# Kernel tuning notes

Measured on AMD Instinct MI355X. Metric: run time of the kernel, lower is better.

## Reference

```python
import jax, jax.numpy as jnp
import numpy as np

# --- configuration (matches pars / init_kwargs) ---
T, B, IN, N = 200, 256, 784, 400
ALPHA, BETA, THRESH = 0.9, 0.8, 1.0          # Synaptic neuron params
BETA_PLUS, BETA_MINUS = 0.9, 0.9             # pre / post trace decay
A_PLUS, A_MINUS = 1e-3, 1e-3                 # classic STDP amplitudes
W_MIN, W_MAX = 0.0, 1.0
LI_STRENGTH = 0.1                            # lateral inhibition strength
SPIKE_RATE = 0.05                            # input Poisson rate per step


def setup_inputs() -> dict:
    key = jax.random.key(0)
    k1, k2 = jax.random.split(key)
    # binary pre-synaptic spike train [T, B, IN]
    image = (jax.random.uniform(k1, (T, B, IN)) < SPIKE_RATE).astype(jnp.float32)
    # torch Linear default init U(-1/sqrt(IN), 1/sqrt(IN)) then clamp to [w_min, w_max]
    bound = 1.0 / np.sqrt(IN)
    W = jnp.clip(jax.random.uniform(k2, (N, IN), minval=-bound, maxval=bound), W_MIN, W_MAX)
    return {"image": image, "W": W}


def _snn_forward(image, W):
    # pre-synaptic traces: traces[0]=0, traces[t+1] = bp*traces[t] + image[t]
    # (STDP at step t uses traces[t], i.e. trace BEFORE incorporating image[t])
    pre_traces = jax.lax.scan(
        lambda tr, x: (BETA_PLUS * tr + x, tr),
        jnp.zeros_like(image[0]), image)[1]            # [T, B, IN]

    batch_ar = jnp.arange(B)

    def step(carry, xs):
        syn, mem, post, W = carry
        img_t, tr_t = xs                               # [B, IN] each
        # fc (no bias)
        cur = img_t @ W.T                              # [B, N]
        # snntorch Synaptic, reset_mechanism='subtract':
        # reset computed from incoming mem, then state update, then fire
        reset = (mem > THRESH).astype(mem.dtype)
        syn = ALPHA * syn + cur
        mem = BETA * mem + syn - reset * THRESH
        spk = (mem > THRESH).astype(mem.dtype)
        mem_rec, spk_rec = mem, spk                    # records taken here
        # lateral inhibition (winner-take-all on syn), skipped if no spikes at all
        win = jnp.argmax(spk, axis=1)                  # first spiking neuron per row
        temp = jnp.ones_like(syn).at[batch_ar, win].set(0.0)
        syn = jnp.where(jnp.sum(spk) > 0, syn - temp * LI_STRENGTH, syn)
        # post-synaptic trace update (STDP uses the UPDATED post trace)
        post = BETA_MINUS * post + spk
        # classic STDP weight update with clamp
        LTP = A_PLUS * (spk.T @ tr_t)                  # [N, IN]
        LTD = A_MINUS * (post.T @ img_t)               # [N, IN]
        W = jnp.clip(W + LTP - LTD, W_MIN, W_MAX)
        return (syn, mem, post, W), (mem_rec, spk_rec)

    zeros = jnp.zeros((B, N), dtype=image.dtype)
    init = (zeros, zeros, zeros, W)
    (_, _, _, W_final), (mem_rec, spk_rec) = jax.lax.scan(step, init, (image, pre_traces))
    return mem_rec, spk_rec, W_final


def reference(image, W):
    # returns (mem record [T,B,N], spike record [T,B,N], final weights [N,IN])
    return _snn_forward(image, W)
```

## Files before the change

### kernel.cpp

```cpp
#include <hip/hip_runtime.h>


#define T_STEPS 200
#define BATCH   256
#define INQ     784
#define NOUT    400
#define NP      512
#define GRID    256
#define NTHR    512
#define IMSZ    200704

#define OFF_WT    0
#define OFF_SYN   401920
#define OFF_MEM   532992
#define OFF_SPPO  664064
#define OFF_TRA   926208
#define OFF_TRB   1126912
#define OFF_WIN   1327616
#define OFF_FLAGS 1327872
#define OFF_BAR   1328128
#define WS_FLOATS 1332224

typedef unsigned long long ull;

__device__ __forceinline__ float ld_coh(const float* p) {
  return __hip_atomic_load(p, __ATOMIC_RELAXED, __HIP_MEMORY_SCOPE_AGENT);
}
__device__ __forceinline__ float2 ld_coh2(const float* p) {
  union { ull u; float2 f; } c;
  c.u = __hip_atomic_load((const ull*)p, __ATOMIC_RELAXED, __HIP_MEMORY_SCOPE_AGENT);
  return c.f;
}
__device__ __forceinline__ void st_coh(float* p, float v) {
  __hip_atomic_store(p, v, __ATOMIC_RELAXED, __HIP_MEMORY_SCOPE_AGENT);
}
__device__ __forceinline__ void st_coh2(float* p, float2 v) {
  union { ull u; float2 f; } c; c.f = v;
  __hip_atomic_store((ull*)p, c.u, __ATOMIC_RELAXED, __HIP_MEMORY_SCOPE_AGENT);
}

__device__ __forceinline__ void gl_lds16(const float* g, float* l) {
  __builtin_amdgcn_global_load_lds(
      (const __attribute__((address_space(1))) void*)g,
      (__attribute__((address_space(3))) void*)l, 16, 0, 0);
}
__device__ __forceinline__ void gl_lds16c(const float* g, float* l) {
  __builtin_amdgcn_global_load_lds(
      (const __attribute__((address_space(1))) void*)g,
      (__attribute__((address_space(3))) void*)l, 16, 0, 0x10);
}

__device__ __forceinline__ void gbar(unsigned* bar, unsigned k, int blk) {
  __syncthreads();
  if (threadIdx.x == 0) {
    const int g = blk >> 3;
    unsigned* garr = bar + g * 64;
    unsigned* ggen = bar + g * 64 + 32;
    unsigned* rarr = bar + 32 * 64;
    unsigned* rgen = bar + 32 * 64 + 32;
    unsigned a = __hip_atomic_fetch_add(garr, 1u, __ATOMIC_RELAXED,
                                        __HIP_MEMORY_SCOPE_AGENT);
    if (a + 1u == k * 8u) {
      unsigned r = __hip_atomic_fetch_add(rarr, 1u, __ATOMIC_RELAXED,
                                          __HIP_MEMORY_SCOPE_AGENT);
      if (r + 1u == k * 32u) {
        __hip_atomic_store(rgen, k, __ATOMIC_RELAXED, __HIP_MEMORY_SCOPE_AGENT);
      } else {
        while (__hip_atomic_load(rgen, __ATOMIC_RELAXED,
                                 __HIP_MEMORY_SCOPE_AGENT) < k)
          __builtin_amdgcn_s_sleep(1);
      }
      __hip_atomic_store(ggen, k, __ATOMIC_RELAXED, __HIP_MEMORY_SCOPE_AGENT);
    } else {
      while (__hip_atomic_load(ggen, __ATOMIC_RELAXED,
                               __HIP_MEMORY_SCOPE_AGENT) < k)
        __builtin_amdgcn_s_sleep(1);
    }
  }
  __syncthreads();
}

__device__ __forceinline__ float clip01(float x) {
  return fminf(fmaxf(x, 0.0f), 1.0f);
}

__global__ void __launch_bounds__(NTHR) snn_kernel(
    const float* __restrict__ img,
    const float* __restrict__ Win,
    float* __restrict__ out,
    float* ws)
{
  float* Wt    = ws + OFF_WT;
  float* syn   = ws + OFF_SYN;
  float* mem   = ws + OFF_MEM;
  float* sppo  = ws + OFF_SPPO;
  float* trA   = ws + OFF_TRA;
  float* trB   = ws + OFF_TRB;
  int*   win   = (int*)(ws + OFF_WIN);
  unsigned* flags = (unsigned*)(ws + OFF_FLAGS);
  unsigned* bar   = (unsigned*)(ws + OFF_BAR);

  float* mem_rec = out;
  float* spk_rec = out + (size_t)T_STEPS * BATCH * NOUT;
  float* Wout    = out + (size_t)2 * T_STEPS * BATCH * NOUT;

  const int tid = threadIdx.x;
  const int blk = blockIdx.x;
  const int wv = tid >> 6, ln = tid & 63;
  unsigned bt = 0;

  __shared__ int   s_list[2][800];
  __shared__ int   s_cnt2[2];
  __shared__ ull   s_msk[13];
  __shared__ int   s_pref[14];
  __shared__ int   s_red8[8];
  __shared__ float stg[3][6144];

  auto build_list = [&](int tt, int slot) {
    const float* row = img + (size_t)tt * IMSZ + (size_t)blk * INQ;
    for (int c = wv; c < 13; c += 8) {
      int i = c * 64 + ln;
      bool act = (i < INQ) && (row[i] != 0.0f);
      ull m = __ballot(act);
      if (ln == 0) s_msk[c] = m;
    }
    __syncthreads();
    if (tid == 0) {
      int acc = 0;
      for (int c = 0; c < 13; ++c) { s_pref[c] = acc; acc += (int)__popcll(s_msk[c]); }
      s_pref[13] = acc;
      int cr = (acc + 15) & ~15;
      if (cr < 48) cr = 48;
      s_cnt2[slot] = cr;
    }
    __syncthreads();
    for (int c = wv; c < 13; c += 8) {
      ull m = s_msk[c];
      if ((m >> ln) & 1ull)
        s_list[slot][s_pref[c] + (int)__popcll(m & ((1ull << ln) - 1ull))] =
            c * 64 + ln;
    }
    int base = s_pref[13];
    int cr = (base + 15) & ~15;
    if (cr < 48) cr = 48;
    if (tid < cr - base) s_list[slot][base + tid] = 784;
  };

  for (int e = blk * NTHR + tid; e < NOUT * INQ; e += GRID * NTHR) {
    int n = e / INQ, i = e % INQ;
    st_coh(Wt + (size_t)i * NP + n, Win[e]);
  }
  build_list(0, 0);
  ++bt; gbar(bar, bt, blk);

  for (int t = 0; t < T_STEPS; ++t) {
    float* trC = (t & 1) ? trB : trA;
    float* trN = (t & 1) ? trA : trB;

    {
      const int b = blk;
      const int slot = t & 1;
      const int cnt = s_cnt2[slot];
      const int anyPrev = (t > 0)
          ? (int)__hip_atomic_load(&flags[t - 1], __ATOMIC_RELAXED, __HIP_MEMORY_SCOPE_AGENT)
          : 0;
      const int wPrev = win[b];
      int localmin = 0x7fffffff;

      if (tid < NOUT) {
        const int n = tid;
        const size_t sidx = (size_t)b * NP + n;
        float2 sp = ld_coh2(sppo + (size_t)b * 1024 + 2 * n);
        float sv = syn[sidx];
        if (anyPrev && n != wPrev) sv -= 0.1f;
        float c0 = 0.f;
        const int* lrow = s_list[slot];
        {
          float q[48];
          #pragma unroll
          for (int u = 0; u < 48; ++u)
            q[u] = ld_coh(Wt + (size_t)lrow[u] * NP + n);
          #pragma unroll
          for (int u = 0; u < 48; ++u) c0 += q[u];
        }
        for (int j = 48; j < cnt; j += 16) {
          float q0  = ld_coh(Wt + (size_t)lrow[j+0]  * NP + n);
          float q1  = ld_coh(Wt + (size_t)lrow[j+1]  * NP + n);
          float q2  = ld_coh(Wt + (size_t)lrow[j+2]  * NP + n);
          float q3  = ld_coh(Wt + (size_t)lrow[j+3]  * NP + n);
          float q4  = ld_coh(Wt + (size_t)lrow[j+4]  * NP + n);
          float q5  = ld_coh(Wt + (size_t)lrow[j+5]  * NP + n);
          float q6  = ld_coh(Wt + (size_t)lrow[j+6]  * NP + n);
          float q7  = ld_coh(Wt + (size_t)lrow[j+7]  * NP + n);
          float q8  = ld_coh(Wt + (size_t)lrow[j+8]  * NP + n);
          float q9  = ld_coh(Wt + (size_t)lrow[j+9]  * NP + n);
          float q10 = ld_coh(Wt + (size_t)lrow[j+10] * NP + n);
          float q11 = ld_coh(Wt + (size_t)lrow[j+11] * NP + n);
          float q12 = ld_coh(Wt + (size_t)lrow[j+12] * NP + n);
          float q13 = ld_coh(Wt + (size_t)lrow[j+13] * NP + n);
          float q14 = ld_coh(Wt + (size_t)lrow[j+14] * NP + n);
          float q15 = ld_coh(Wt + (size_t)lrow[j+15] * NP + n);
          c0 += q0;  c0 += q1;  c0 += q2;  c0 += q3;
          c0 += q4;  c0 += q5;  c0 += q6;  c0 += q7;
          c0 += q8;  c0 += q9;  c0 += q10; c0 += q11;
          c0 += q12; c0 += q13; c0 += q14; c0 += q15;
        }
        float mv = mem[sidx];
        float syn0 = fmaf(0.9f, sv, c0);
        float r0 = (mv > 1.0f) ? 1.0f : 0.0f;
        float m0 = fmaf(0.8f, mv, syn0) - r0;
        float s0 = (m0 > 1.0f) ? 1.0f : 0.0f;
        syn[sidx] = syn0;
        mem[sidx] = m0;
        float p0 = fmaf(0.9f, sp.y, s0);
        st_coh2(sppo + (size_t)b * 1024 + 2 * n, make_float2(s0, p0));
        const size_t ridx = (size_t)t * BATCH * NOUT + (size_t)b * NOUT + n;
        mem_rec[ridx] = m0;
        spk_rec[ridx] = s0;
        if (s0 != 0.f) localmin = n;
      }
      int v = localmin;
      #pragma unroll
      for (int s = 1; s < 64; s <<= 1) v = min(v, __shfl_xor(v, s));
      if (ln == 0) s_red8[wv] = v;
      __syncthreads();
      if (tid == 0) {
        int w = s_red8[0];
        #pragma unroll
        for (int q = 1; q < 8; ++q) w = min(w, s_red8[q]);
        win[b] = (w == 0x7fffffff) ? 0 : w;
        if (w != 0x7fffffff)
          __hip_atomic_fetch_or(&flags[t], 1u, __ATOMIC_RELAXED, __HIP_MEMORY_SCOPE_AGENT);
      }
    }
    ++bt; gbar(bar, bt, blk);

    const float* imrow  = img + (size_t)t * IMSZ + (size_t)blk * INQ;
    const float* trCrow = trC + (size_t)blk * INQ;
    float*       trNrow = trN + (size_t)blk * INQ;
    const bool hasTr = (tid * 2 < INQ);
    float2 tro = make_float2(0.f, 0.f), tiv = tro;
    if (hasTr) {
      tro = ld_coh2(trCrow + tid * 2);
      tiv = *(const float2*)(imrow + tid * 2);
    }

    if (blk < 169) {
      const int bi = blk / 13, bn = blk % 13;
      const int ib0 = bi * 64, nb0 = bn * 32;
      const int brow0 = wv * 4 + (ln >> 4);
      int icol = ib0 + (ln & 15) * 4;
      if (icol > INQ - 4) icol = INQ - 4;
      const int scol = 2 * nb0 + ((ln & 15) ^ ((ln >> 4) & 1)) * 4;
      const float* imgt = img + (size_t)t * BATCH * INQ;

      const int h  = ln >> 5;
      const int il = (ln & 31) >> 2;
      const int nl = ln & 3;
      const int wb = wv * 256;

      const int cc = tid & 31;
      const int kb = (tid >> 5) * 4;
      const int iiO = kb >> 3, j0 = kb & 7;
      const int ilO = cc >> 2, nlO = cc & 3;
      const int i_loc = (iiO < 4) ? (ilO * 4 + iiO) : (32 + ilO * 4 + (iiO - 4));
      const int iO = ib0 + i_loc;
      const int nO = nb0 + nlO * 8 + j0;
      const bool okO = (nO < NOUT) && (iO < INQ);
      float2 wA = make_float2(0.f, 0.f), wB = wA;
      if (okO) {
        wA = ld_coh2(Wt + (size_t)iO * NP + nO);
        wB = ld_coh2(Wt + (size_t)iO * NP + nO + 2);
      }

      float a[8][8] = {};

      #define STG(c, buf) {                                                     \
        int br = (c) * 32 + brow0;                                              \
        float* dst = &stg[buf][wb];                                             \
        gl_lds16c(trC  + (size_t)br * INQ  + icol, dst);                        \
        gl_lds16 (imgt + (size_t)br * INQ  + icol, dst + 2048);                 \
        gl_lds16c(sppo + (size_t)br * 1024 + scol, dst + 4096);                 \
      }

      STG(0, 0);
      STG(1, 1);
      for (int c = 0; c < 8; ++c) {
        const int buf = c % 3;
        if (c + 2 < 8) {
          STG(c + 2, (c + 2) % 3);
          __builtin_amdgcn_s_waitcnt(0x0F76);
        } else if (c == 6) {
          __builtin_amdgcn_s_waitcnt(0x0F73);
        } else {
          __builtin_amdgcn_s_waitcnt(0x0F70);
        }
        #pragma unroll
        for (int qr = 0; qr < 2; ++qr) {
          const int r  = 2 * qr + h;
          const int rb = wb + r * 64;
          const float4 t0 = *(const float4*)&stg[buf][rb + il * 4];
          const float4 t1 = *(const float4*)&stg[buf][rb + 32 + il * 4];
          const float4 g0 = *(const float4*)&stg[buf][2048 + rb + il * 4];
          const float4 g1 = *(const float4*)&stg[buf][2048 + rb + 32 + il * 4];
          const int sb = 4096 + rb;
          const float4 s0 = *(const float4*)&stg[buf][sb + (((nl * 4 + 0) ^ h) << 2)];
          const float4 s1 = *(const float4*)&stg[buf][sb + (((nl * 4 + 1) ^ h) << 2)];
          const float4 s2 = *(const float4*)&stg[buf][sb + (((nl * 4 + 2) ^ h) << 2)];
          const float4 s3 = *(const float4*)&stg[buf][sb + (((nl * 4 + 3) ^ h) << 2)];
          const float tv[8] = { t0.x, t0.y, t0.z, t0.w, t1.x, t1.y, t1.z, t1.w };
          const float gv[8] = { g0.x, g0.y, g0.z, g0.w, g1.x, g1.y, g1.z, g1.w };
          const float ap[8] = { 1e-3f * s0.x, 1e-3f * s0.z, 1e-3f * s1.x, 1e-3f * s1.z,
                                1e-3f * s2.x, 1e-3f * s2.z, 1e-3f * s3.x, 1e-3f * s3.z };
          const float am[8] = { 1e-3f * s0.y, 1e-3f * s0.w, 1e-3f * s1.y, 1e-3f * s1.w,
                                1e-3f * s2.y, 1e-3f * s2.w, 1e-3f * s3.y, 1e-3f * s3.w };
          #pragma unroll
          for (int ii = 0; ii < 8; ++ii)
            #pragma unroll
            for (int j = 0; j < 8; ++j)
              a[ii][j] = fmaf(tv[ii], ap[j], fmaf(gv[ii], -am[j], a[ii][j]));
        }
      }
      #undef STG

      __syncthreads();

      float* part = &stg[0][0];
      float dsum[4];

      if (wv < 4) {
        #pragma unroll
        for (int ii = 0; ii < 8; ++ii)
          #pragma unroll
          for (int j = 0; j < 8; ++j)
            part[wv * 4096 + (ii * 8 + j) * 64 + ln] = a[ii][j];
      }
      __syncthreads();
      #pragma unroll
      for (int kk = 0; kk < 4; ++kk) {
        const int k = kb + kk;
        float s0 = part[0 * 4096 + k * 64 + cc] + part[0 * 4096 + k * 64 + cc + 32];
        float s1 = part[1 * 4096 + k * 64 + cc] + part[1 * 4096 + k * 64 + cc + 32];
        float s2 = part[2 * 4096 + k * 64 + cc] + part[2 * 4096 + k * 64 + cc + 32];
        float s3 = part[3 * 4096 + k * 64 + cc] + part[3 * 4096 + k * 64 + cc + 32];
        dsum[kk] = ((s0 + s1) + s2) + s3;
      }
      __syncthreads();
      if (wv >= 4) {
        #pragma unroll
        for (int ii = 0; ii < 8; ++ii)
          #pragma unroll
          for (int j = 0; j < 8; ++j)
            part[(wv - 4) * 4096 + (ii * 8 + j) * 64 + ln] = a[ii][j];
      }
      __syncthreads();
      #pragma unroll
      for (int kk = 0; kk < 4; ++kk) {
        const int k = kb + kk;
        float s0 = part[0 * 4096 + k * 64 + cc] + part[0 * 4096 + k * 64 + cc + 32];
        float s1 = part[1 * 4096 + k * 64 + cc] + part[1 * 4096 + k * 64 + cc + 32];
        float s2 = part[2 * 4096 + k * 64 + cc] + part[2 * 4096 + k * 64 + cc + 32];
        float s3 = part[3 * 4096 + k * 64 + cc] + part[3 * 4096 + k * 64 + cc + 32];
        dsum[kk] += ((s0 + s1) + s2) + s3;
      }

      if (okO) {
        wA.x = clip01(wA.x + dsum[0]);
        wA.y = clip01(wA.y + dsum[1]);
        st_coh2(Wt + (size_t)iO * NP + nO, wA);
        wB.x = clip01(wB.x + dsum[2]);
        wB.y = clip01(wB.y + dsum[3]);
        st_coh2(Wt + (size_t)iO * NP + nO + 2, wB);
      }
    }

    if (hasTr)
      st_coh2(trNrow + tid * 2, make_float2(fmaf(0.9f, tro.x, tiv.x),
                                            fmaf(0.9f, tro.y, tiv.y)));
    if (t + 1 < T_STEPS) build_list(t + 1, (t + 1) & 1);

    ++bt; gbar(bar, bt, blk);
  }

  for (int e = blk * NTHR + tid; e < NOUT * INQ; e += GRID * NTHR) {
    int n = e / INQ, i = e % INQ;
    Wout[e] = ld_coh(Wt + (size_t)i * NP + n);
  }
}

extern "C" void kernel_launch(void* const* d_in, const int* in_sizes, int n_in,
                              void* d_out, int out_size, void* d_ws, size_t ws_size,
                              hipStream_t stream) {
  const float* img = (const float*)d_in[0];
  const float* W   = (const float*)d_in[1];
  float* out = (float*)d_out;
  float* ws  = (float*)d_ws;

  hipMemsetAsync(d_ws, 0, (size_t)WS_FLOATS * sizeof(float), stream);

  void* args[] = { (void*)&img, (void*)&W, (void*)&out, (void*)&ws };
  hipLaunchCooperativeKernel((const void*)snn_kernel, dim3(GRID), dim3(NTHR),
                             args, 0, stream);
}
```

Before: 4.184 ms.

## Build next spike list in idle wave and flatten grid barrier wait

The active-input list for the next timestep is now built by one otherwise idle wavefront (wave 7) inside the forward phase, using register ballots instead of shared masks and two block syncs. Before, it ran after the STDP phase, just before the grid barrier. The hierarchical barrier now has every block spin on the single root generation word rather than a per-group word. The aim is to cut serial sync work on the critical path between barriers. In exchange, all 256 blocks now poll one shared address, which adds contention on that word.

After: 3.878 ms. 7.3% less time.

```diff
diff --git a/kernel.cpp b/kernel.cpp
--- a/kernel.cpp
+++ b/kernel.cpp
@@ -54,28 +54,18 @@
   __syncthreads();
   if (threadIdx.x == 0) {
     const int g = blk >> 3;
-    unsigned* garr = bar + g * 64;
-    unsigned* ggen = bar + g * 64 + 32;
-    unsigned* rarr = bar + 32 * 64;
     unsigned* rgen = bar + 32 * 64 + 32;
-    unsigned a = __hip_atomic_fetch_add(garr, 1u, __ATOMIC_RELAXED,
+    unsigned a = __hip_atomic_fetch_add(bar + g * 64, 1u, __ATOMIC_RELAXED,
                                         __HIP_MEMORY_SCOPE_AGENT);
     if (a + 1u == k * 8u) {
-      unsigned r = __hip_atomic_fetch_add(rarr, 1u, __ATOMIC_RELAXED,
+      unsigned r = __hip_atomic_fetch_add(bar + 32 * 64, 1u, __ATOMIC_RELAXED,
                                           __HIP_MEMORY_SCOPE_AGENT);
-      if (r + 1u == k * 32u) {
+      if (r + 1u == k * 32u)
         __hip_atomic_store(rgen, k, __ATOMIC_RELAXED, __HIP_MEMORY_SCOPE_AGENT);
-      } else {
-        while (__hip_atomic_load(rgen, __ATOMIC_RELAXED,
-                                 __HIP_MEMORY_SCOPE_AGENT) < k)
-          __builtin_amdgcn_s_sleep(1);
-      }
-      __hip_atomic_store(ggen, k, __ATOMIC_RELAXED, __HIP_MEMORY_SCOPE_AGENT);
-    } else {
-      while (__hip_atomic_load(ggen, __ATOMIC_RELAXED,
-                               __HIP_MEMORY_SCOPE_AGENT) < k)
-        __builtin_amdgcn_s_sleep(1);
-    }
+    }
+    while (__hip_atomic_load(rgen, __ATOMIC_RELAXED,
+                             __HIP_MEMORY_SCOPE_AGENT) < k)
+      __builtin_amdgcn_s_sleep(1);
   }
   __syncthreads();
 }
@@ -111,46 +101,42 @@
 
   __shared__ int   s_list[2][800];
   __shared__ int   s_cnt2[2];
-  __shared__ ull   s_msk[13];
-  __shared__ int   s_pref[14];
   __shared__ int   s_red8[8];
   __shared__ float stg[3][6144];
 
-  auto build_list = [&](int tt, int slot) {
+  auto build_list_w7 = [&](int tt, int slot) {
     const float* row = img + (size_t)tt * IMSZ + (size_t)blk * INQ;
-    for (int c = wv; c < 13; c += 8) {
+    float v[13];
+    #pragma unroll
+    for (int c = 0; c < 13; ++c) {
       int i = c * 64 + ln;
-      bool act = (i < INQ) && (row[i] != 0.0f);
-      ull m = __ballot(act);
-      if (ln == 0) s_msk[c] = m;
-    }
-    __syncthreads();
-    if (tid == 0) {
-      int acc = 0;
-      for (int c = 0; c < 13; ++c) { s_pref[c] = acc; acc += (int)__popcll(s_msk[c]); }
-      s_pref[13] = acc;
-      int cr = (acc + 15) & ~15;
-      if (cr < 48) cr = 48;
-      s_cnt2[slot] = cr;
-    }
-    __syncthreads();
-    for (int c = wv; c < 13; c += 8) {
-      ull m = s_msk[c];
-      if ((m >> ln) & 1ull)
-        s_list[slot][s_pref[c] + (int)__popcll(m & ((1ull << ln) - 1ull))] =
+      v[c] = row[(i < INQ) ? i : (INQ - 1)];
+    }
+    ull m[13];
+    #pragma unroll
+    for (int c = 0; c < 13; ++c) {
+      int i = c * 64 + ln;
+      m[c] = __ballot((i < INQ) && (v[c] != 0.0f));
+    }
+    int base = 0;
+    #pragma unroll
+    for (int c = 0; c < 13; ++c) {
+      if ((m[c] >> ln) & 1ull)
+        s_list[slot][base + (int)__popcll(m[c] & ((1ull << ln) - 1ull))] =
             c * 64 + ln;
-    }
-    int base = s_pref[13];
+      base += (int)__popcll(m[c]);
+    }
     int cr = (base + 15) & ~15;
     if (cr < 48) cr = 48;
-    if (tid < cr - base) s_list[slot][base + tid] = 784;
+    if (ln < cr - base) s_list[slot][base + ln] = 784;
+    if (ln == 0) s_cnt2[slot] = cr;
   };
 
   for (int e = blk * NTHR + tid; e < NOUT * INQ; e += GRID * NTHR) {
     int n = e / INQ, i = e % INQ;
     st_coh(Wt + (size_t)i * NP + n, Win[e]);
   }
-  build_list(0, 0);
+  if (wv == 7) build_list_w7(0, 0);
   ++bt; gbar(bar, bt, blk);
 
   for (int t = 0; t < T_STEPS; ++t) {
@@ -167,7 +153,9 @@
       const int wPrev = win[b];
       int localmin = 0x7fffffff;
 
-      if (tid < NOUT) {
+      if (wv == 7) {
+        if (t + 1 < T_STEPS) build_list_w7(t + 1, (t + 1) & 1);
+      } else if (tid < NOUT) {
         const int n = tid;
         const size_t sidx = (size_t)b * NP + n;
         float2 sp = ld_coh2(sppo + (size_t)b * 1024 + 2 * n);
@@ -219,15 +207,17 @@
         spk_rec[ridx] = s0;
         if (s0 != 0.f) localmin = n;
       }
-      int v = localmin;
-      #pragma unroll
-      for (int s = 1; s < 64; s <<= 1) v = min(v, __shfl_xor(v, s));
-      if (ln == 0) s_red8[wv] = v;
+      if (wv < 7) {
+        int v = localmin;
+        #pragma unroll
+        for (int s = 1; s < 64; s <<= 1) v = min(v, __shfl_xor(v, s));
+        if (ln == 0) s_red8[wv] = v;
+      }
       __syncthreads();
       if (tid == 0) {
         int w = s_red8[0];
         #pragma unroll
-        for (int q = 1; q < 8; ++q) w = min(w, s_red8[q]);
+        for (int q = 1; q < 7; ++q) w = min(w, s_red8[q]);
         win[b] = (w == 0x7fffffff) ? 0 : w;
         if (w != 0x7fffffff)
           __hip_atomic_fetch_or(&flags[t], 1u, __ATOMIC_RELAXED, __HIP_MEMORY_SCOPE_AGENT);
@@ -377,7 +367,6 @@
     if (hasTr)
       st_coh2(trNrow + tid * 2, make_float2(fmaf(0.9f, tro.x, tiv.x),
                                             fmaf(0.9f, tro.y, tiv.y)));
-    if (t + 1 < T_STEPS) build_list(t + 1, (t + 1) & 1);
 
     ++bt; gbar(bar, bt, blk);
   }
```
